# Optimization experiments

Measured on AMD Instinct MI355X. Metric: run time of the kernel, lower is better.

## Reference

```python
import jax, jax.numpy as jnp
import numpy as np

TRAIN_COUNT, FEAT = 20000, 40
BATCH, NN, M = 2048, 64, 10


def _safe_l2(d2):
    # sqrt with zero (not NaN/inf) gradient at d2 == 0 (diagonal of pairwise dists)
    pos = d2 > 0
    return jnp.where(pos, jnp.sqrt(jnp.where(pos, d2, 1.0)), 0.0)


def setup_inputs() -> dict:
    key = jax.random.key(0)
    k1, k2, k3, k4 = jax.random.split(key, 4)
    x = jax.random.normal(k1, (TRAIN_COUNT, FEAT), dtype=jnp.float32)
    batch_indices = jax.random.randint(k2, (BATCH,), 0, TRAIN_COUNT)
    batch_nn_indices = jax.random.randint(k3, (BATCH, NN), 0, TRAIN_COUNT)
    batch_nn_targets = jax.random.normal(k4, (BATCH, NN, M), dtype=jnp.float32)
    length_scale = jnp.ones((M,), dtype=jnp.float32)
    eps = 1e-3 * jnp.ones((M,), dtype=jnp.float32)
    return {
        "x": x,
        "length_scale": length_scale,
        "eps": eps,
        "batch_indices": batch_indices,
        "batch_nn_indices": batch_nn_indices,
        "batch_nn_targets": batch_nn_targets,
    }


def reference(x, length_scale, eps, batch_indices, batch_nn_indices, batch_nn_targets):
    b, nn, m = batch_nn_targets.shape
    xb = x[batch_indices]          # (b, f)
    xn = x[batch_nn_indices]       # (b, nn, f)

    # crosswise l2 distances (b, nn)
    cd = _safe_l2(jnp.sum((xb[:, None, :] - xn) ** 2, axis=-1))
    # pairwise l2 distances (b, nn, nn)
    pd = _safe_l2(jnp.sum((xn[:, :, None, :] - xn[:, None, :, :]) ** 2, axis=-1))

    # Matern nu = 1/2: k(d) = exp(-d / length_scale); vectorized over the m models
    Kcross = jnp.exp(-cd[None, :, :] / length_scale[:, None, None])            # (m, b, nn)
    K = jnp.exp(-pd[None, :, :, :] / length_scale[:, None, None, None])        # (m, b, nn, nn)
    eye = jnp.eye(nn, dtype=K.dtype)
    Kp = K + eps[:, None, None, None] * eye                                     # homoscedastic perturb

    Y = jnp.moveaxis(batch_nn_targets, -1, 0)[..., None]                        # (m, b, nn, 1)
    F = jnp.linalg.solve(Kp, Y)[..., 0]                                         # (m, b, nn)
    predictions = jnp.einsum("mbn,mbn->bm", Kcross, F)

    G = jnp.linalg.solve(Kp, Kcross[..., None])[..., 0]                         # (m, b, nn)
    variances = 1.0 - jnp.einsum("mbn,mbn->bm", Kcross, G)

    sigma_sq = jnp.sum(Y[..., 0] * F, axis=(1, 2)) / (b * nn)                   # (m,)
    return predictions, variances, sigma_sq
```

## Files before the change

### kernel.cpp

```cpp
#include <hip/hip_runtime.h>
#include <math.h>

#define BATCH 2048
#define NN 64
#define FEAT 40
#define M 10
#define NPAIR 32
#define PPAD 34

__device__ __forceinline__ float rl(float v, int l) {
    return __int_as_float(__builtin_amdgcn_readlane(__float_as_int(v), l));
}
__device__ __forceinline__ int rli(int v, int l) {
    return __builtin_amdgcn_readlane(v, l);
}
__device__ __forceinline__ float wsum(float v) {
#pragma unroll
    for (int o = 32; o >= 1; o >>= 1) v += __shfl_xor(v, o, 64);
    return v;
}

__global__ __launch_bounds__(64)
__attribute__((amdgpu_waves_per_eu(2, 2)))
void muygps_kernel(
    const float* __restrict__ x,
    const float* __restrict__ ls,
    const float* __restrict__ epsv,
    const int*   __restrict__ bidx,
    const int*   __restrict__ nidx,
    const float* __restrict__ tgt,
    float* __restrict__ out,
    float* __restrict__ ws)
{
    __shared__ float2 Ap[PPAD * NN];

    const int b    = blockIdx.x;
    const int lane = threadIdx.x;

    const int nv = nidx[b * NN + lane];
    const float* xr0 = x + (size_t)nv * FEAT;
    float xc[FEAT];
#pragma unroll
    for (int q = 0; q < FEAT / 4; ++q) {
        const float4 v = *(const float4*)(xr0 + 4 * q);
        xc[4*q] = v.x; xc[4*q+1] = v.y; xc[4*q+2] = v.z; xc[4*q+3] = v.w;
    }
    float nl = 0.f;
#pragma unroll
    for (int f = 0; f < FEAT; ++f) nl = fmaf(xc[f], xc[f], nl);

    const float* xbp = x + (size_t)bidx[b] * FEAT;
    float gc = 0.f, nb = 0.f;
#pragma unroll
    for (int f = 0; f < FEAT; ++f) {
        const float bf = xbp[f];
        gc = fmaf(bf, xc[f], gc);
        nb = fmaf(bf, bf, nb);
    }
    float cd2 = (nb + nl) - 2.f * gc;
    cd2 = (cd2 < 0.05f) ? 0.f : cd2;
    const float cdv = sqrtf(cd2);

    unsigned done = 0;
    const unsigned all = (1u << M) - 1u;
    while (true) {
        const int   lead = __ffs(~done) - 1;
        const float lls  = ls[lead];
        const float lep  = epsv[lead];
        const float il   = -1.0f / lls;

#pragma unroll 2
        for (int i = 0; i < NN; i += 2) {
            const int ri0 = rli(nv, i), ri1 = rli(nv, i + 1);
            const float* r0 = x + (size_t)ri0 * FEAT;
            const float* r1 = x + (size_t)ri1 * FEAT;
            float g0 = 0.f, g1 = 0.f;
#pragma unroll
            for (int f = 0; f < FEAT; ++f) {
                g0 = fmaf(r0[f], xc[f], g0);
                g1 = fmaf(r1[f], xc[f], g1);
            }
            float d2a = (rl(g0, i) + nl) - 2.f * g0;
            float d2b = (rl(g1, i + 1) + nl) - 2.f * g1;
            d2a = (d2a < 0.05f) ? 0.f : d2a;
            d2b = (d2b < 0.05f) ? 0.f : d2b;
            float va = __expf(sqrtf(d2a) * il);
            float vb = __expf(sqrtf(d2b) * il);
            if (lane == i)     va += lep;
            if (lane == i + 1) vb += lep;
            Ap[(i >> 1) * NN + lane] = float2{va, vb};
        }
        const float kcv = __expf(cdv * il);

        float z[M + 1];
        z[0] = kcv;
        {
            const float* trow = tgt + ((size_t)b * NN + lane) * M;
#pragma unroll
            for (int q = 0; q < M / 2; ++q) {
                const float2 v = *(const float2*)(trow + 2 * q);
                z[2 * q + 1] = v.x; z[2 * q + 2] = v.y;
            }
        }

        float2 pv = Ap[lane];
        float pc0 = pv.x, pc1 = pv.y;
        float2 nn2 = Ap[NN + lane];
        float n2 = nn2.x, n3 = nn2.y;
        float rvv = 0.f;
        for (int p = 0; p < 31; ++p) {
            const int k = 2 * p;
            const float2 V = Ap[(p + 2) * NN + lane];
            float2 U = Ap[(p + 3) * NN + lane];
            const float d0  = rl(pc0, k);
            const float r0  = __builtin_amdgcn_rcpf(d0);
            const float cv0 = pc0 * (-r0);
            pc1 = fmaf(cv0, rl(pc0, k + 1), pc1);
            const float d1  = rl(pc1, k + 1);
            const float r1  = __builtin_amdgcn_rcpf(d1);
            const float cv1 = pc1 * (-r1);
            rvv = (lane == k)     ? r0 : rvv;
            rvv = (lane == k + 1) ? r1 : rvv;
            const float lv0 = (lane > k)     ? cv0 : 0.f;
            const float lv1 = (lane > k + 1) ? cv1 : 0.f;
#pragma unroll
            for (int j = 0; j < M + 1; ++j) {
                z[j] = fmaf(lv0, rl(z[j], k), z[j]);
                z[j] = fmaf(lv1, rl(z[j], k + 1), z[j]);
            }
            const float t2 = fmaf(cv1, rl(pc1, k + 2), fmaf(cv0, rl(pc0, k + 2), n2));
            const float t3 = fmaf(cv1, rl(pc1, k + 3), fmaf(cv0, rl(pc0, k + 3), n3));
            n2 = fmaf(cv1, rl(pc1, k + 4), fmaf(cv0, rl(pc0, k + 4), V.x));
            n3 = fmaf(cv1, rl(pc1, k + 5), fmaf(cv0, rl(pc0, k + 5), V.y));
#pragma unroll 2
            for (int q = p + 3; q < NPAIR; ++q) {
                float2 cur = U;
                U = Ap[(q + 1) * NN + lane];
                const int i0 = 2 * q;
                cur.x = fmaf(cv0, rl(pc0, i0),     fmaf(cv1, rl(pc1, i0),     cur.x));
                cur.y = fmaf(cv0, rl(pc0, i0 + 1), fmaf(cv1, rl(pc1, i0 + 1), cur.y));
                Ap[q * NN + lane] = cur;
            }
            pc0 = t2; pc1 = t3;
        }
        {
            const float d0  = rl(pc0, 62);
            const float r0  = __builtin_amdgcn_rcpf(d0);
            const float cv0 = pc0 * (-r0);
            pc1 = fmaf(cv0, rl(pc0, 63), pc1);
            const float d1  = rl(pc1, 63);
            const float r1  = __builtin_amdgcn_rcpf(d1);
            rvv = (lane == 62) ? r0 : rvv;
            rvv = (lane == 63) ? r1 : rvv;
            const float lv0 = (lane > 62) ? cv0 : 0.f;
#pragma unroll
            for (int j = 0; j < M + 1; ++j)
                z[j] = fmaf(lv0, rl(z[j], 62), z[j]);
        }

        const float zc  = z[0];
        const float quad = wsum(zc * zc * rvv);
        unsigned mb = 0;
#pragma unroll
        for (int m = 0; m < M; ++m)
            if (!(done & (1u << m)) && ls[m] == lls && epsv[m] == lep)
                mb |= 1u << m;
        float predv = 0.f, sigv = 0.f;
#pragma unroll
        for (int m = 0; m < M; ++m) {
            if (mb & (1u << m)) {
                const float zm = z[m + 1];
                const float pm = wsum(zc * zm * rvv);
                const float sm = wsum(zm * zm * rvv);
                if (lane == m) { predv = pm; sigv = sm; }
            }
        }
        if (lane < M && ((mb >> lane) & 1u)) {
            out[b * M + lane] = predv;
            out[BATCH * M + b * M + lane] = 1.0f - quad;
            ws[lane * BATCH + b] = sigv;
        }
        done |= mb;
        if (done == all) break;
    }
}

__global__ __launch_bounds__(640)
void sigma_reduce(const float* __restrict__ ws, float* __restrict__ out) {
    const int w = threadIdx.x >> 6, lane = threadIdx.x & 63;
    const float4* p = (const float4*)(ws + w * BATCH);
    float a = 0.f;
#pragma unroll
    for (int i = 0; i < BATCH / 4 / 64; ++i) {
        const float4 v = p[i * 64 + lane];
        a += (v.x + v.y) + (v.z + v.w);
    }
    a = wsum(a);
    if (lane == 0)
        out[2 * BATCH * M + w] = a * (1.0f / (float)(BATCH * NN));
}

extern "C" void kernel_launch(void* const* d_in, const int* in_sizes, int n_in,
                              void* d_out, int out_size, void* d_ws, size_t ws_size,
                              hipStream_t stream) {
    const float* x   = (const float*)d_in[0];
    const float* lsp = (const float*)d_in[1];
    const float* ep  = (const float*)d_in[2];
    const int*   bi  = (const int*)d_in[3];
    const int*   ni  = (const int*)d_in[4];
    const float* tg  = (const float*)d_in[5];
    float* out = (float*)d_out;
    float* ws  = (float*)d_ws;

    muygps_kernel<<<BATCH, 64, 0, stream>>>(x, lsp, ep, bi, ni, tg, out, ws);
    sigma_reduce<<<1, 640, 0, stream>>>(ws, out);
}
```

Before: 141.9 us.

## Split each batch item's Cholesky solve across two wavefronts

Each block now runs two wavefronts instead of one. The wavefronts split the pairwise-kernel row construction in half, and they split the trailing-update rows of the LDL elimination using a per-step partition. Wave 1 alone handles the right-hand-side solves and the reductions. This adds a __syncthreads per elimination step and duplicates the pivot-row math in both waves. The aim is to cut the latency of each serial factorisation by parallelising the row updates, in exchange for barrier overhead and some redundant work.

```diff
diff --git a/kernel.cpp b/kernel.cpp
--- a/kernel.cpp
+++ b/kernel.cpp
@@ -20,8 +20,8 @@
     return v;
 }
 
-__global__ __launch_bounds__(64)
-__attribute__((amdgpu_waves_per_eu(2, 2)))
+__global__ __launch_bounds__(128)
+__attribute__((amdgpu_waves_per_eu(4, 4)))
 void muygps_kernel(
     const float* __restrict__ x,
     const float* __restrict__ ls,
@@ -35,7 +35,8 @@
     __shared__ float2 Ap[PPAD * NN];
 
     const int b    = blockIdx.x;
-    const int lane = threadIdx.x;
+    const int w    = threadIdx.x >> 6;
+    const int lane = threadIdx.x & 63;
 
     const int nv = nidx[b * NN + lane];
     const float* xr0 = x + (size_t)nv * FEAT;
@@ -49,17 +50,20 @@
 #pragma unroll
     for (int f = 0; f < FEAT; ++f) nl = fmaf(xc[f], xc[f], nl);
 
-    const float* xbp = x + (size_t)bidx[b] * FEAT;
-    float gc = 0.f, nb = 0.f;
-#pragma unroll
-    for (int f = 0; f < FEAT; ++f) {
-        const float bf = xbp[f];
-        gc = fmaf(bf, xc[f], gc);
-        nb = fmaf(bf, bf, nb);
-    }
-    float cd2 = (nb + nl) - 2.f * gc;
-    cd2 = (cd2 < 0.05f) ? 0.f : cd2;
-    const float cdv = sqrtf(cd2);
+    float cdv = 0.f;
+    if (w == 1) {
+        const float* xbp = x + (size_t)bidx[b] * FEAT;
+        float gc = 0.f, nb = 0.f;
+#pragma unroll
+        for (int f = 0; f < FEAT; ++f) {
+            const float bf = xbp[f];
+            gc = fmaf(bf, xc[f], gc);
+            nb = fmaf(bf, bf, nb);
+        }
+        float cd2 = (nb + nl) - 2.f * gc;
+        cd2 = (cd2 < 0.05f) ? 0.f : cd2;
+        cdv = sqrtf(cd2);
+    }
 
     unsigned done = 0;
     const unsigned all = (1u << M) - 1u;
@@ -69,39 +73,46 @@
         const float lep  = epsv[lead];
         const float il   = -1.0f / lls;
 
+        {
+            const int r0b = w << 5;
 #pragma unroll 2
-        for (int i = 0; i < NN; i += 2) {
-            const int ri0 = rli(nv, i), ri1 = rli(nv, i + 1);
-            const float* r0 = x + (size_t)ri0 * FEAT;
-            const float* r1 = x + (size_t)ri1 * FEAT;
-            float g0 = 0.f, g1 = 0.f;
-#pragma unroll
-            for (int f = 0; f < FEAT; ++f) {
-                g0 = fmaf(r0[f], xc[f], g0);
-                g1 = fmaf(r1[f], xc[f], g1);
-            }
-            float d2a = (rl(g0, i) + nl) - 2.f * g0;
-            float d2b = (rl(g1, i + 1) + nl) - 2.f * g1;
-            d2a = (d2a < 0.05f) ? 0.f : d2a;
-            d2b = (d2b < 0.05f) ? 0.f : d2b;
-            float va = __expf(sqrtf(d2a) * il);
-            float vb = __expf(sqrtf(d2b) * il);
-            if (lane == i)     va += lep;
-            if (lane == i + 1) vb += lep;
-            Ap[(i >> 1) * NN + lane] = float2{va, vb};
-        }
-        const float kcv = __expf(cdv * il);
+            for (int it = 0; it < 32; it += 2) {
+                const int i = r0b + it;
+                const int ri0 = rli(nv, i), ri1 = rli(nv, i + 1);
+                const float* r0 = x + (size_t)ri0 * FEAT;
+                const float* r1 = x + (size_t)ri1 * FEAT;
+                float g0 = 0.f, g1 = 0.f;
+#pragma unroll
+                for (int f = 0; f < FEAT; ++f) {
+                    g0 = fmaf(r0[f], xc[f], g0);
+                    g1 = fmaf(r1[f], xc[f], g1);
+                }
+                float d2a = (rl(g0, i) + nl) - 2.f * g0;
+                float d2b = (rl(g1, i + 1) + nl) - 2.f * g1;
+                d2a = (d2a < 0.05f) ? 0.f : d2a;
+                d2b = (d2b < 0.05f) ? 0.f : d2b;
+                float va = __expf(sqrtf(d2a) * il);
+                float vb = __expf(sqrtf(d2b) * il);
+                if (lane == i)     va += lep;
+                if (lane == i + 1) vb += lep;
+                Ap[(i >> 1) * NN + lane] = float2{va, vb};
+            }
+        }
 
         float z[M + 1];
-        z[0] = kcv;
-        {
+        if (w == 1) {
+            z[0] = __expf(cdv * il);
             const float* trow = tgt + ((size_t)b * NN + lane) * M;
 #pragma unroll
             for (int q = 0; q < M / 2; ++q) {
                 const float2 v = *(const float2*)(trow + 2 * q);
                 z[2 * q + 1] = v.x; z[2 * q + 2] = v.y;
             }
-        }
+        } else {
+#pragma unroll
+            for (int j = 0; j < M + 1; ++j) z[j] = 0.f;
+        }
+        __syncthreads();
 
         float2 pv = Ap[lane];
         float pc0 = pv.x, pc1 = pv.y;
@@ -110,8 +121,8 @@
         float rvv = 0.f;
         for (int p = 0; p < 31; ++p) {
             const int k = 2 * p;
+            const int qs = p + 3;
             const float2 V = Ap[(p + 2) * NN + lane];
-            float2 U = Ap[(p + 3) * NN + lane];
             const float d0  = rl(pc0, k);
             const float r0  = __builtin_amdgcn_rcpf(d0);
             const float cv0 = pc0 * (-r0);
@@ -121,27 +132,36 @@
             const float cv1 = pc1 * (-r1);
             rvv = (lane == k)     ? r0 : rvv;
             rvv = (lane == k + 1) ? r1 : rvv;
-            const float lv0 = (lane > k)     ? cv0 : 0.f;
-            const float lv1 = (lane > k + 1) ? cv1 : 0.f;
-#pragma unroll
-            for (int j = 0; j < M + 1; ++j) {
-                z[j] = fmaf(lv0, rl(z[j], k), z[j]);
-                z[j] = fmaf(lv1, rl(z[j], k + 1), z[j]);
+            if (w == 1) {
+                const float lv0 = (lane > k)     ? cv0 : 0.f;
+                const float lv1 = (lane > k + 1) ? cv1 : 0.f;
+#pragma unroll
+                for (int j = 0; j < M + 1; ++j) {
+                    z[j] = fmaf(lv0, rl(z[j], k), z[j]);
+                    z[j] = fmaf(lv1, rl(z[j], k + 1), z[j]);
+                }
             }
             const float t2 = fmaf(cv1, rl(pc1, k + 2), fmaf(cv0, rl(pc0, k + 2), n2));
             const float t3 = fmaf(cv1, rl(pc1, k + 3), fmaf(cv0, rl(pc0, k + 3), n3));
             n2 = fmaf(cv1, rl(pc1, k + 4), fmaf(cv0, rl(pc0, k + 4), V.x));
             n3 = fmaf(cv1, rl(pc1, k + 5), fmaf(cv0, rl(pc0, k + 5), V.y));
-#pragma unroll 2
-            for (int q = p + 3; q < NPAIR; ++q) {
-                float2 cur = U;
-                U = Ap[(q + 1) * NN + lane];
-                const int i0 = 2 * q;
-                cur.x = fmaf(cv0, rl(pc0, i0),     fmaf(cv1, rl(pc1, i0),     cur.x));
-                cur.y = fmaf(cv0, rl(pc0, i0 + 1), fmaf(cv1, rl(pc1, i0 + 1), cur.y));
-                Ap[q * NN + lane] = cur;
+            const int rem = NPAIR - qs;
+            int W1 = rem / 2 - 2; if (W1 < 0) W1 = 0;
+            const int lo = (w == 0) ? qs : NPAIR - W1;
+            const int hi = (w == 0) ? NPAIR - W1 : NPAIR;
+            if (lo < hi) {
+                float2 U = Ap[lo * NN + lane];
+                for (int q = lo; q < hi; ++q) {
+                    float2 cur = U;
+                    U = Ap[(q + 1) * NN + lane];
+                    const int i0 = 2 * q;
+                    cur.x = fmaf(cv0, rl(pc0, i0),     fmaf(cv1, rl(pc1, i0),     cur.x));
+                    cur.y = fmaf(cv0, rl(pc0, i0 + 1), fmaf(cv1, rl(pc1, i0 + 1), cur.y));
+                    Ap[q * NN + lane] = cur;
+                }
             }
             pc0 = t2; pc1 = t3;
+            __syncthreads();
         }
         {
             const float d0  = rl(pc0, 62);
@@ -152,36 +172,41 @@
             const float r1  = __builtin_amdgcn_rcpf(d1);
             rvv = (lane == 62) ? r0 : rvv;
             rvv = (lane == 63) ? r1 : rvv;
-            const float lv0 = (lane > 62) ? cv0 : 0.f;
-#pragma unroll
-            for (int j = 0; j < M + 1; ++j)
-                z[j] = fmaf(lv0, rl(z[j], 62), z[j]);
-        }
-
-        const float zc  = z[0];
-        const float quad = wsum(zc * zc * rvv);
+            if (w == 1) {
+                const float lv0 = (lane > 62) ? cv0 : 0.f;
+#pragma unroll
+                for (int j = 0; j < M + 1; ++j)
+                    z[j] = fmaf(lv0, rl(z[j], 62), z[j]);
+            }
+        }
+
         unsigned mb = 0;
 #pragma unroll
         for (int m = 0; m < M; ++m)
             if (!(done & (1u << m)) && ls[m] == lls && epsv[m] == lep)
                 mb |= 1u << m;
-        float predv = 0.f, sigv = 0.f;
-#pragma unroll
-        for (int m = 0; m < M; ++m) {
-            if (mb & (1u << m)) {
-                const float zm = z[m + 1];
-                const float pm = wsum(zc * zm * rvv);
-                const float sm = wsum(zm * zm * rvv);
-                if (lane == m) { predv = pm; sigv = sm; }
-            }
-        }
-        if (lane < M && ((mb >> lane) & 1u)) {
-            out[b * M + lane] = predv;
-            out[BATCH * M + b * M + lane] = 1.0f - quad;
-            ws[lane * BATCH + b] = sigv;
+        if (w == 1) {
+            const float zc  = z[0];
+            const float quad = wsum(zc * zc * rvv);
+            float predv = 0.f, sigv = 0.f;
+#pragma unroll
+            for (int m = 0; m < M; ++m) {
+                if (mb & (1u << m)) {
+                    const float zm = z[m + 1];
+                    const float pm = wsum(zc * zm * rvv);
+                    const float sm = wsum(zm * zm * rvv);
+                    if (lane == m) { predv = pm; sigv = sm; }
+                }
+            }
+            if (lane < M && ((mb >> lane) & 1u)) {
+                out[b * M + lane] = predv;
+                out[BATCH * M + b * M + lane] = 1.0f - quad;
+                ws[lane * BATCH + b] = sigv;
+            }
         }
         done |= mb;
         if (done == all) break;
+        __syncthreads();
     }
 }
 
@@ -212,6 +237,6 @@
     float* out = (float*)d_out;
     float* ws  = (float*)d_ws;
 
-    muygps_kernel<<<BATCH, 64, 0, stream>>>(x, lsp, ep, bi, ni, tg, out, ws);
+    muygps_kernel<<<BATCH, 128, 0, stream>>>(x, lsp, ep, bi, ni, tg, out, ws);
     sigma_reduce<<<1, 640, 0, stream>>>(ws, out);
 }
```

After: 151.4 us. 6.7% more time.
